# Kernel tuning notes

Measured on AMD Instinct MI355X. Metric: run time of the kernel, lower is better.

The kernel has to match this reference:

```python
import jax, jax.numpy as jnp
import numpy as np

N_HEAD = 16
N_FEAT = 1024
D_HEAD = N_FEAT // N_HEAD


def setup_inputs() -> dict:
    key = jax.random.key(0)
    ks = jax.random.split(key, 12)
    B, L, T = 8, 128, 64
    s = 0.05
    return {
        "q": jax.random.normal(ks[0], (B, 1, N_FEAT), jnp.float32),
        "kv": jax.random.normal(ks[1], (B, L, T, N_FEAT), jnp.float32),
        "Wq": jax.random.normal(ks[2], (D_HEAD, D_HEAD), jnp.float32) * s,
        "bq": jax.random.normal(ks[3], (D_HEAD,), jnp.float32) * s,
        "Wk": jax.random.normal(ks[4], (D_HEAD, D_HEAD), jnp.float32) * s,
        "bk": jax.random.normal(ks[5], (D_HEAD,), jnp.float32) * s,
        "Wv": jax.random.normal(ks[6], (D_HEAD, D_HEAD), jnp.float32) * s,
        "bv": jax.random.normal(ks[7], (D_HEAD,), jnp.float32) * s,
        "Wo": jax.random.normal(ks[8], (N_FEAT, N_FEAT), jnp.float32) * s,
        "bo": jax.random.normal(ks[9], (N_FEAT,), jnp.float32) * s,
    }


def reference(q, kv, Wq, bq, Wk, bk, Wv, bv, Wo, bo):
    B, L, T, D = kv.shape
    H, dh = N_HEAD, D_HEAD
    # mean-pool q over its singleton length dim and kv over T for keys
    qm = q.mean(axis=-2)                      # [B, D]
    km = kv.mean(axis=-2)                     # [B, L, D]
    qh = qm.reshape(B, H, dh)                 # [B, H, dh]
    kh = km.reshape(B, L, H, dh)              # [B, L, H, dh]
    vh = kv.reshape(B, L, T, H, dh)           # [B, L, T, H, dh]
    # per-head linear projections (torch Linear: x @ W.T + b)
    qh = qh @ Wq.T + bq
    kh = kh @ Wk.T + bk
    vh = vh @ Wv.T + bv
    # faithful transpose chain from the original module
    qh = jnp.swapaxes(qh, -2, -3)             # [H, B, dh]  (3D: swaps B and H)
    kh = jnp.swapaxes(kh, -2, -3)             # [B, H, L, dh]
    # broadcasted matmul -> cross-batch attention [B, H, B, L]
    attw = jnp.matmul(qh, jnp.swapaxes(kh, -1, -2)) / jnp.sqrt(jnp.float32(dh))
    attn = jax.nn.softmax(attw, axis=-1)      # [B, H, B, L]
    # value reshuffle: [B,L,T,H,dh] -> [B,H,T,L,dh] -> [B,H,T,dh,L] -> [B,H,T*dh,L]
    v = jnp.swapaxes(vh, -2, -4)
    v = jnp.swapaxes(v, -1, -2)
    v = v.reshape(B, H, T * dh, L)
    ct = jnp.matmul(attn, jnp.swapaxes(v, -1, -2))   # [B, H, B, T*dh]
    ct = ct.reshape(B, H, B, T, dh)
    ct = jnp.swapaxes(ct, -2, -4)                    # [B, T, B, H, dh]
    ct = ct.reshape(B, T, B, H * dh)                 # [B, T, B, D]
    return ct @ Wo.T + bo
```

## Files before the change

kernel.cpp:

```cpp
#include <hip/hip_runtime.h>
#include <hip/hip_bf16.h>

#define BDIM 8
#define LDIM 128
#define TDIM 64
#define NFEAT 1024
#define HNUM 16
#define DH 64

#define GM 4096
#define GN 1024
#define GK 1024

typedef __attribute__((ext_vector_type(8))) short short8;
typedef __attribute__((ext_vector_type(4))) float f32x4;

__device__ __forceinline__ unsigned short f2bf(float x) {
  union { float f; unsigned u; } v; v.f = x;
  unsigned r = v.u + 0x7fffu + ((v.u >> 16) & 1u);
  return (unsigned short)(r >> 16);
}

__device__ __forceinline__ void gload_lds16(const void* g, void* l) {
  __builtin_amdgcn_global_load_lds((const __attribute__((address_space(1))) void*)g,
                                   (__attribute__((address_space(3))) void*)l, 16, 0, 0);
}

__global__ __launch_bounds__(256) void mean_score_weff_kernel(
    const float* __restrict__ kv, const float* __restrict__ q,
    const float* __restrict__ Wq, const float* __restrict__ bq,
    const float* __restrict__ Wk, const float* __restrict__ Wo,
    const float* __restrict__ Wv, const float* __restrict__ bv,
    const float* __restrict__ bo, float* __restrict__ scores,
    unsigned short* __restrict__ Weff, float* __restrict__ beff) {
  __shared__ float km_s[NFEAT];
  __shared__ float Wk_s[DH * 67];
  __shared__ float kw_s[HNUM * DH];
  __shared__ float wqkw_s[HNUM * 66];
  __shared__ float bqkw_s[HNUM];
  __shared__ float worow[NFEAT];
  __shared__ float red[256];
  const int bl = blockIdx.x;
  const int tid = threadIdx.x;

  {
    const float* src = kv + (size_t)bl * (TDIM * NFEAT) + tid * 4;
    float4 acc = make_float4(0.f, 0.f, 0.f, 0.f);
    for (int t0 = 0; t0 < TDIM; t0 += 8) {
      float4 v[8];
#pragma unroll
      for (int jj = 0; jj < 8; ++jj)
        v[jj] = *(const float4*)(src + (t0 + jj) * NFEAT);
#pragma unroll
      for (int jj = 0; jj < 8; ++jj) {
        acc.x += v[jj].x; acc.y += v[jj].y; acc.z += v[jj].z; acc.w += v[jj].w;
      }
    }
    const float s = 1.f / TDIM;
    *(float4*)(km_s + tid * 4) = make_float4(acc.x * s, acc.y * s, acc.z * s, acc.w * s);
  }
#pragma unroll
  for (int rep = 0; rep < 4; ++rep) {
    const int e4 = rep * 256 + tid;
    const int row = e4 >> 4, c4 = e4 & 15;
    const float4 v = *(const float4*)(Wk + row * DH + c4 * 4);
    float* dst = Wk_s + row * 67 + c4 * 4;
    dst[0] = v.x; dst[1] = v.y; dst[2] = v.z; dst[3] = v.w;
  }
  __syncthreads();
#pragma unroll
  for (int rep = 0; rep < 4; ++rep) {
    const int e = rep * 256 + tid;
    const int h = e >> 6, dd = e & 63;
    float acc = 0.f;
#pragma unroll 4
    for (int d = 0; d < DH; ++d) acc += Wk_s[dd * 67 + d] * km_s[h * 64 + d];
    kw_s[h * 64 + dd] = acc;
  }
  __syncthreads();
#pragma unroll
  for (int rep = 0; rep < 4; ++rep) {
    const int e = rep * 256 + tid;
    const int h = e >> 6, i = e & 63;
    float acc = 0.f;
#pragma unroll 4
    for (int dd = 0; dd < DH; ++dd) acc += Wq[dd * DH + i] * kw_s[h * 64 + dd];
    wqkw_s[h * 66 + i] = acc;
  }
  if (tid < HNUM) {
    float acc = 0.f;
#pragma unroll 4
    for (int dd = 0; dd < DH; ++dd) acc += bq[dd] * kw_s[tid * 64 + dd];
    bqkw_s[tid] = acc;
  }
  __syncthreads();
  {
    const int w = tid >> 6, lane = tid & 63;
    for (int k = 0; k < 32; ++k) {
      const int e = w * 32 + k;
      const int h = e >> 3, b2 = e & 7;
      float p = q[b2 * NFEAT + h * DH + lane] * wqkw_s[h * 66 + lane];
#pragma unroll
      for (int s = 1; s < 64; s <<= 1) p += __shfl_xor(p, s, 64);
      if (lane == 0) scores[(size_t)bl * 128 + e] = (p + bqkw_s[h]) * 0.125f;
    }
  }
  {
    const int f = bl;
    *(float4*)(worow + tid * 4) = *(const float4*)(Wo + (size_t)f * NFEAT + tid * 4);
    __syncthreads();
    const int g0 = tid * 4;
    const int hbase = (g0 >> 6) << 6;
    const int i0 = g0 & 63;
    float a0 = 0, a1 = 0, a2 = 0, a3 = 0;
#pragma unroll 4
    for (int d = 0; d < DH; ++d) {
      const float wod = worow[hbase + d];
      const float4 wv4 = *(const float4*)(Wv + d * DH + i0);
      a0 += wod * wv4.x; a1 += wod * wv4.y; a2 += wod * wv4.z; a3 += wod * wv4.w;
    }
    ushort4 pk;
    pk.x = f2bf(a0); pk.y = f2bf(a1); pk.z = f2bf(a2); pk.w = f2bf(a3);
    *(ushort4*)(Weff + (size_t)f * NFEAT + g0) = pk;
    red[tid] = worow[g0 + 0] * bv[i0 + 0] + worow[g0 + 1] * bv[i0 + 1] +
               worow[g0 + 2] * bv[i0 + 2] + worow[g0 + 3] * bv[i0 + 3];
    __syncthreads();
    for (int sft = 128; sft > 0; sft >>= 1) {
      if (tid < sft) red[tid] += red[tid + sft];
      __syncthreads();
    }
    if (tid == 0) beff[f] = bo[f] + red[0];
  }
}

__global__ __launch_bounds__(64) void pool_kernel(
    const float* __restrict__ kv, const float* __restrict__ scores,
    unsigned short* __restrict__ pooled) {
  __shared__ float wldsT[LDIM * 36];
  __shared__ float mrow[32], irow[32];
  const int b1 = blockIdx.x;
  const int t = blockIdx.y;
  const int ftile = blockIdx.z;
  const int tid = threadIdx.x;
  const float* sc = scores + (size_t)b1 * (LDIM * 128) + ftile * 32;
  {
    const int hb = tid & 31, half = tid >> 5;
    const float* scp = sc + (size_t)(half * 64) * 128 + hb;
    float m = -1e30f;
    for (int j = 0; j < 64; ++j) m = fmaxf(m, scp[j * 128]);
    m = fmaxf(m, __shfl_xor(m, 32, 64));
    float ssum = 0.f;
    for (int j = 0; j < 64; ++j) ssum += expf(scp[j * 128] - m);
    ssum += __shfl_xor(ssum, 32, 64);
    if (half == 0) { mrow[hb] = m; irow[hb] = 1.f / ssum; }
  }
  __syncthreads();
  for (int rep = 0; rep < 64; ++rep) {
    const int e = rep * 64 + tid;
    const int hb = e & 31, l = e >> 5;
    wldsT[l * 36 + hb] = expf(sc[(size_t)l * 128 + hb] - mrow[hb]) * irow[hb];
  }
  __syncthreads();
  const int f = ftile * 256 + tid * 4;
  const int hh = tid >> 4;
  const float* kvbase = kv + ((size_t)b1 * LDIM) * (TDIM * NFEAT) + t * NFEAT + f;
  float4 acc[8];
#pragma unroll
  for (int b2 = 0; b2 < 8; ++b2) acc[b2] = make_float4(0.f, 0.f, 0.f, 0.f);
  for (int l0 = 0; l0 < LDIM; l0 += 8) {
    float4 v[8];
#pragma unroll
    for (int j = 0; j < 8; ++j)
      v[j] = *(const float4*)(kvbase + (size_t)(l0 + j) * (TDIM * NFEAT));
#pragma unroll
    for (int j = 0; j < 8; ++j) {
      const float* wrow = wldsT + (l0 + j) * 36 + hh * 8;
#pragma unroll
      for (int b2 = 0; b2 < 8; ++b2) {
        const float w = wrow[b2];
        acc[b2].x += w * v[j].x; acc[b2].y += w * v[j].y;
        acc[b2].z += w * v[j].z; acc[b2].w += w * v[j].w;
      }
    }
  }
  unsigned short* obase = pooled + ((size_t)(b1 * TDIM + t) * BDIM) * NFEAT + f;
#pragma unroll
  for (int b2 = 0; b2 < 8; ++b2) {
    ushort4 pk;
    pk.x = f2bf(acc[b2].x); pk.y = f2bf(acc[b2].y);
    pk.z = f2bf(acc[b2].z); pk.w = f2bf(acc[b2].w);
    *(ushort4*)(obase + b2 * NFEAT) = pk;
  }
}

__global__ __launch_bounds__(256) void mfma_gemm(const unsigned short* __restrict__ A,
                                                 const unsigned short* __restrict__ W,
                                                 const float* __restrict__ beff,
                                                 float* __restrict__ out) {
  __shared__ unsigned short As[2][128 * 32];
  __shared__ unsigned short Bs[2][64 * 32];
  const int tid = threadIdx.x;
  const int w = tid >> 6, l = tid & 63;
  const int mBase = blockIdx.y * 128, nBase = blockIdx.x * 64;
  const int wr = w >> 1, wc = w & 1;

  int arow[2], acol[2];
#pragma unroll
  for (int j = 0; j < 2; ++j) {
    const int cid = j * 256 + tid;
    const int r = cid >> 2, c = cid & 3;
    arow[j] = r;
    acol[j] = (c ^ ((r >> 1) & 3)) * 8;
  }
  const int brow = tid >> 2;
  const int bcol = ((tid & 3) ^ ((brow >> 1) & 3)) * 8;

  const int rl = l & 15, ks = l >> 4;
  const int fsel = (ks ^ ((rl >> 1) & 3)) * 16;

  f32x4 acc[4][2] = {};

#pragma unroll
  for (int j = 0; j < 2; ++j)
    gload_lds16(A + (size_t)(mBase + arow[j]) * GK + acol[j],
                (char*)As[0] + (j * 256 + tid) * 16);
  gload_lds16(W + (size_t)(nBase + brow) * GK + bcol, (char*)Bs[0] + tid * 16);
  __syncthreads();

  int cur = 0;
  for (int t = 0; t < GK / 32; ++t) {
    if (t + 1 < GK / 32) {
      const int k0 = (t + 1) * 32;
#pragma unroll
      for (int j = 0; j < 2; ++j)
        gload_lds16(A + (size_t)(mBase + arow[j]) * GK + k0 + acol[j],
                    (char*)As[cur ^ 1] + (j * 256 + tid) * 16);
      gload_lds16(W + (size_t)(nBase + brow) * GK + k0 + bcol,
                  (char*)Bs[cur ^ 1] + tid * 16);
    }
    short8 a[4], b[2];
#pragma unroll
    for (int m = 0; m < 4; ++m)
      a[m] = *(const short8*)((const char*)As[cur] + (wr * 64 + m * 16 + rl) * 64 + fsel);
#pragma unroll
    for (int n = 0; n < 2; ++n)
      b[n] = *(const short8*)((const char*)Bs[cur] + (wc * 32 + n * 16 + rl) * 64 + fsel);
#pragma unroll
    for (int m = 0; m < 4; ++m)
#pragma unroll
      for (int n = 0; n < 2; ++n)
        acc[m][n] = __builtin_amdgcn_mfma_f32_16x16x32_bf16(a[m], b[n], acc[m][n], 0, 0, 0);
    __syncthreads();
    cur ^= 1;
  }

#pragma unroll
  for (int n = 0; n < 2; ++n) {
    const int col = nBase + wc * 32 + n * 16 + rl;
    const float bv = beff[col];
#pragma unroll
    for (int m = 0; m < 4; ++m) {
      const int row0 = mBase + wr * 64 + m * 16 + ks * 4;
#pragma unroll
      for (int j2 = 0; j2 < 4; ++j2)
        out[(size_t)(row0 + j2) * GN + col] = acc[m][n][j2] + bv;
    }
  }
}

extern "C" void kernel_launch(void* const* d_in, const int* in_sizes, int n_in,
                              void* d_out, int out_size, void* d_ws, size_t ws_size,
                              hipStream_t stream) {
  const float* q  = (const float*)d_in[0];
  const float* kv = (const float*)d_in[1];
  const float* Wq = (const float*)d_in[2];
  const float* bq = (const float*)d_in[3];
  const float* Wk = (const float*)d_in[4];
  const float* Wv = (const float*)d_in[6];
  const float* bv = (const float*)d_in[7];
  const float* Wo = (const float*)d_in[8];
  const float* bo = (const float*)d_in[9];
  float* out = (float*)d_out;

  char* ws = (char*)d_ws;
  float*          scores = (float*)ws;
  float*          beff   = (float*)(ws + (1u << 20));
  unsigned short* Weff   = (unsigned short*)(ws + (1u << 20) + (4u << 10));
  unsigned short* pooled = (unsigned short*)(ws + (4u << 20));

  mean_score_weff_kernel<<<BDIM * LDIM, 256, 0, stream>>>(
      kv, q, Wq, bq, Wk, Wo, Wv, bv, bo, scores, Weff, beff);
  pool_kernel<<<dim3(BDIM, TDIM, 4), 64, 0, stream>>>(kv, scores, pooled);
  mfma_gemm<<<dim3(GN / 64, GM / 128), 256, 0, stream>>>(pooled, Weff, beff, out);
}
```

Measured before the change: 156.5 us.

## Store scores L-contiguous and compute softmax from registers in pool kernel

Scores are now written in [b1,h,b2,l] order, so the softmax in the pool kernel reads each row as contiguous float4 loads, keeps the exponentials in registers and writes normalized weights to LDS in one pass. The strided score reads and the second expf pass are gone. The score dot product also changes from a 64-lane shuffle reduction per element to one thread per (h,b2) doing a float4 dot product. In exchange the LDS weight reads in the inner loop become strided by LDIM per b2 rather than contiguous, which may cause bank conflicts or more LDS instructions.

```diff
diff --git a/kernel.cpp b/kernel.cpp
--- a/kernel.cpp
+++ b/kernel.cpp
@@ -42,6 +42,7 @@
   __shared__ float red[256];
   const int bl = blockIdx.x;
   const int tid = threadIdx.x;
+  const int b1 = bl >> 7, l = bl & 127;
 
   {
     const float* src = kv + (size_t)bl * (TDIM * NFEAT) + tid * 4;
@@ -94,16 +95,19 @@
     bqkw_s[tid] = acc;
   }
   __syncthreads();
-  {
-    const int w = tid >> 6, lane = tid & 63;
-    for (int k = 0; k < 32; ++k) {
-      const int e = w * 32 + k;
-      const int h = e >> 3, b2 = e & 7;
-      float p = q[b2 * NFEAT + h * DH + lane] * wqkw_s[h * 66 + lane];
-#pragma unroll
-      for (int s = 1; s < 64; s <<= 1) p += __shfl_xor(p, s, 64);
-      if (lane == 0) scores[(size_t)bl * 128 + e] = (p + bqkw_s[h]) * 0.125f;
-    }
+  if (tid < 128) {
+    const int h = tid >> 3, b2 = tid & 7;
+    const float* qrow = q + b2 * NFEAT + h * DH;
+    const float* wrow = wqkw_s + h * 66;
+    float acc = 0.f;
+#pragma unroll
+    for (int i4 = 0; i4 < 16; ++i4) {
+      const float4 qv = *(const float4*)(qrow + i4 * 4);
+      acc += qv.x * wrow[i4 * 4 + 0] + qv.y * wrow[i4 * 4 + 1] +
+             qv.z * wrow[i4 * 4 + 2] + qv.w * wrow[i4 * 4 + 3];
+    }
+    scores[(((size_t)b1 * HNUM + h) * BDIM + b2) * LDIM + l] =
+        (acc + bqkw_s[h]) * 0.125f;
   }
   {
     const int f = bl;
@@ -133,32 +137,44 @@
   }
 }
 
+#define HSTRIDE 1032
 __global__ __launch_bounds__(64) void pool_kernel(
     const float* __restrict__ kv, const float* __restrict__ scores,
     unsigned short* __restrict__ pooled) {
-  __shared__ float wldsT[LDIM * 36];
-  __shared__ float mrow[32], irow[32];
+  __shared__ float wlds[4 * HSTRIDE];
   const int b1 = blockIdx.x;
   const int t = blockIdx.y;
   const int ftile = blockIdx.z;
   const int tid = threadIdx.x;
-  const float* sc = scores + (size_t)b1 * (LDIM * 128) + ftile * 32;
   {
-    const int hb = tid & 31, half = tid >> 5;
-    const float* scp = sc + (size_t)(half * 64) * 128 + hb;
+    const int row = tid & 31;
+    const int half = tid >> 5;
+    const int hloc = row >> 3, b2 = row & 7;
+    const float* srow = scores +
+        (((size_t)b1 * HNUM + ftile * 4 + hloc) * BDIM + b2) * LDIM + half * 64;
+    float4 sv[16];
+#pragma unroll
+    for (int j = 0; j < 16; ++j) sv[j] = *(const float4*)(srow + j * 4);
     float m = -1e30f;
-    for (int j = 0; j < 64; ++j) m = fmaxf(m, scp[j * 128]);
+#pragma unroll
+    for (int j = 0; j < 16; ++j)
+      m = fmaxf(m, fmaxf(fmaxf(sv[j].x, sv[j].y), fmaxf(sv[j].z, sv[j].w)));
     m = fmaxf(m, __shfl_xor(m, 32, 64));
     float ssum = 0.f;
-    for (int j = 0; j < 64; ++j) ssum += expf(scp[j * 128] - m);
+#pragma unroll
+    for (int j = 0; j < 16; ++j) {
+      sv[j].x = expf(sv[j].x - m); sv[j].y = expf(sv[j].y - m);
+      sv[j].z = expf(sv[j].z - m); sv[j].w = expf(sv[j].w - m);
+      ssum += sv[j].x + sv[j].y + sv[j].z + sv[j].w;
+    }
     ssum += __shfl_xor(ssum, 32, 64);
-    if (half == 0) { mrow[hb] = m; irow[hb] = 1.f / ssum; }
-  }
-  __syncthreads();
-  for (int rep = 0; rep < 64; ++rep) {
-    const int e = rep * 64 + tid;
-    const int hb = e & 31, l = e >> 5;
-    wldsT[l * 36 + hb] = expf(sc[(size_t)l * 128 + hb] - mrow[hb]) * irow[hb];
+    const float inv = 1.f / ssum;
+    float* wdst = wlds + hloc * HSTRIDE + b2 * LDIM + half * 64;
+#pragma unroll
+    for (int j = 0; j < 16; ++j) {
+      float4 w4 = make_float4(sv[j].x * inv, sv[j].y * inv, sv[j].z * inv, sv[j].w * inv);
+      *(float4*)(wdst + j * 4) = w4;
+    }
   }
   __syncthreads();
   const int f = ftile * 256 + tid * 4;
@@ -167,6 +183,7 @@
   float4 acc[8];
 #pragma unroll
   for (int b2 = 0; b2 < 8; ++b2) acc[b2] = make_float4(0.f, 0.f, 0.f, 0.f);
+  const float* wbase = wlds + hh * HSTRIDE;
   for (int l0 = 0; l0 < LDIM; l0 += 8) {
     float4 v[8];
 #pragma unroll
@@ -174,10 +191,9 @@
       v[j] = *(const float4*)(kvbase + (size_t)(l0 + j) * (TDIM * NFEAT));
 #pragma unroll
     for (int j = 0; j < 8; ++j) {
-      const float* wrow = wldsT + (l0 + j) * 36 + hh * 8;
 #pragma unroll
       for (int b2 = 0; b2 < 8; ++b2) {
-        const float w = wrow[b2];
+        const float w = wbase[b2 * LDIM + l0 + j];
         acc[b2].x += w * v[j].x; acc[b2].y += w * v[j].y;
         acc[b2].z += w * v[j].z; acc[b2].w += w * v[j].w;
       }
```

Result: faster. 138.7 us (-11.3%).
